# Kernel tuning notes

Measured on AMD Instinct MI355X. Metric: run time of the kernel, lower is better.

The kernel has to match this reference:

```python
import jax, jax.numpy as jnp
import numpy as np

DIM = 256; K = 3; PAD = 1; DIL = 1; B = 16; H = 56; W = 56
SP = 8           # share_planes
RADIX = 2
ATTN = max(DIM * RADIX // 4, 32)   # 128
EMB = K * K * DIM // SP            # 288

def conv(x, w, pad=0, dil=1, groups=1):
    return jax.lax.conv_general_dilated(
        x, w, (1, 1), [(pad, pad), (pad, pad)], rhs_dilation=(dil, dil),
        feature_group_count=groups, dimension_numbers=('NCHW', 'OIHW', 'NCHW'))

def bn(x, g, b, m, v, eps=1e-5):
    # eval-mode BatchNorm2d
    s = g * jax.lax.rsqrt(v + eps)
    return x * s[None, :, None, None] + (b - m * s)[None, :, None, None]

def gn(x, g, b, groups, eps=1e-5):
    Bb, C, Hh, Ww = x.shape
    xg = x.reshape(Bb, groups, C // groups, Hh, Ww)
    mu = xg.mean((2, 3, 4), keepdims=True)
    var = xg.var((2, 3, 4), keepdims=True)
    xg = (xg - mu) * jax.lax.rsqrt(var + eps)
    return xg.reshape(Bb, C, Hh, Ww) * g[None, :, None, None] + b[None, :, None, None]

def unfold3(x):
    # im2col for 3x3, stride 1, pad 1 -> (B, C, K*K, H, W)
    Bb, C, Hh, Ww = x.shape
    p = (K - 1) // 2
    xp = jnp.pad(x, ((0, 0), (0, 0), (p, p), (p, p)))
    return jnp.stack([xp[:, :, i:i + Hh, j:j + Ww] for i in range(K) for j in range(K)], axis=2)

def reference(x, ke_w, ke_g, ke_b, ke_m, ke_v, e1_w, e1_g, e1_b, e1_m, e1_v,
              e2_w, e2_b, gng, gnb, c1_w, c1_g, c1_b, c1_m, c1_v,
              b2_g, b2_b, b2_m, b2_v, s1_w, s1_b, s1_g, s1_bb, s1_m, s1_v,
              s2_w, s2_b):
    Bb = x.shape[0]
    # key embed: grouped kxk conv + BN + ReLU
    k = jax.nn.relu(bn(conv(x, ke_w, pad=PAD, dil=DIL, groups=4), ke_g, ke_b, ke_m, ke_v))
    qk = jnp.concatenate([x, k], axis=1)                     # (B, 2*DIM, H, W)
    # dynamic kernel branch
    wemb = jax.nn.relu(bn(conv(qk, e1_w), e1_g, e1_b, e1_m, e1_v))
    wemb = conv(wemb, e2_w) + e2_b[None, :, None, None]
    wemb = gn(wemb, gng, gnb, DIM // SP)                     # GroupNorm(dim//8 groups)
    wemb = wemb.reshape(Bb, DIM // SP, K * K, H, W)
    # value branch
    xq = bn(conv(x, c1_w), c1_g, c1_b, c1_m, c1_v)
    # local dynamic convolution: per-pixel kernel shared across SP channels
    patches = unfold3(xq).reshape(Bb, DIM // SP, SP, K * K, H, W)
    y = (patches * wemb[:, :, None]).sum(3).reshape(Bb, DIM, H, W)
    y = bn(y, b2_g, b2_b, b2_m, b2_v)
    y = y * jax.nn.sigmoid(y)                                # swish
    # split attention over radix=2 branches (y, k)
    xs = jnp.stack([y, k], axis=2)                           # (B, C, 2, H, W)
    gap = xs.sum(2).mean((2, 3), keepdims=True)              # (B, C, 1, 1)
    a = jax.nn.relu(bn(conv(gap, s1_w) + s1_b[None, :, None, None], s1_g, s1_bb, s1_m, s1_v))
    a = conv(a, s2_w) + s2_b[None, :, None, None]            # (B, 2*C, 1, 1)
    a = jax.nn.softmax(a.reshape(Bb, DIM, RADIX), axis=2)
    out = (xs * a[:, :, :, None, None]).sum(2)
    return out

def setup_inputs():
    key = jax.random.key(0)
    ks = iter(jax.random.split(key, 40))
    def n(shape, s=1.0):
        return jax.random.normal(next(ks), shape, jnp.float32) * s
    def u(shape):
        return jax.random.uniform(next(ks), shape, jnp.float32, minval=0.5, maxval=1.5)
    d = {}
    d['x'] = n((B, DIM, H, W))
    d['ke_w'] = n((DIM, DIM // 4, K, K), 0.05)
    d['ke_g'] = u((DIM,)); d['ke_b'] = n((DIM,), 0.1); d['ke_m'] = n((DIM,), 0.1); d['ke_v'] = u((DIM,))
    d['e1_w'] = n((DIM // 2, 2 * DIM, 1, 1), 0.05)
    d['e1_g'] = u((DIM // 2,)); d['e1_b'] = n((DIM // 2,), 0.1); d['e1_m'] = n((DIM // 2,), 0.1); d['e1_v'] = u((DIM // 2,))
    d['e2_w'] = n((EMB, DIM // 2, 1, 1), 0.05); d['e2_b'] = n((EMB,), 0.1)
    d['gng'] = u((EMB,)); d['gnb'] = n((EMB,), 0.1)
    d['c1_w'] = n((DIM, DIM, 1, 1), 0.05)
    d['c1_g'] = u((DIM,)); d['c1_b'] = n((DIM,), 0.1); d['c1_m'] = n((DIM,), 0.1); d['c1_v'] = u((DIM,))
    d['b2_g'] = u((DIM,)); d['b2_b'] = n((DIM,), 0.1); d['b2_m'] = n((DIM,), 0.1); d['b2_v'] = u((DIM,))
    d['s1_w'] = n((ATTN, DIM, 1, 1), 0.05); d['s1_b'] = n((ATTN,), 0.1)
    d['s1_g'] = u((ATTN,)); d['s1_bb'] = n((ATTN,), 0.1); d['s1_m'] = n((ATTN,), 0.1); d['s1_v'] = u((ATTN,))
    d['s2_w'] = n((RADIX * DIM, ATTN, 1, 1), 0.05); d['s2_b'] = n((RADIX * DIM,), 0.1)
    return d
```

## Files before the change

### kernel.cpp

```cpp
#include <hip/hip_runtime.h>
#include <hip/hip_bf16.h>

typedef __hip_bfloat16 bf16;
typedef float f32x4 __attribute__((ext_vector_type(4)));
typedef short s16x8 __attribute__((ext_vector_type(8)));

#define NPIX 3136
#define HDIM 56
#define CDIM 256

static __device__ __forceinline__ float b2f(bf16 v){ return __bfloat162float(v); }
static __device__ __forceinline__ bf16  f2b(float v){ return __float2bfloat16(v); }

#define O_KE_S 0
#define O_KE_B 256
#define O_E1_S 512
#define O_E1_B 640
#define O_C1_S 768
#define O_C1_B 1024
#define O_B2_S 1280
#define O_B2_B 1536
#define O_S1_S 1792
#define O_S1_B 1920
#define O_E2B  2048
#define O_GN_MU 2336
#define O_GN_RS 2848
#define O_GAP   3360
#define O_ATT   7456

__global__ void fold_params(
    const float* keg, const float* keb, const float* kem, const float* kev,
    const float* e1g, const float* e1b, const float* e1m, const float* e1v,
    const float* e2b,
    const float* c1g, const float* c1b, const float* c1m, const float* c1v,
    const float* b2g, const float* b2b, const float* b2m, const float* b2v,
    const float* s1g, const float* s1bb, const float* s1m, const float* s1v,
    float* o)
{
    int t = threadIdx.x;
    const float eps = 1e-5f;
    if (t < 256) {
        float s = keg[t] * rsqrtf(kev[t] + eps);
        o[O_KE_S + t] = s; o[O_KE_B + t] = keb[t] - kem[t] * s;
        s = c1g[t] * rsqrtf(c1v[t] + eps);
        o[O_C1_S + t] = s; o[O_C1_B + t] = c1b[t] - c1m[t] * s;
        s = b2g[t] * rsqrtf(b2v[t] + eps);
        o[O_B2_S + t] = s; o[O_B2_B + t] = b2b[t] - b2m[t] * s;
    }
    if (t < 128) {
        float s = e1g[t] * rsqrtf(e1v[t] + eps);
        o[O_E1_S + t] = s; o[O_E1_B + t] = e1b[t] - e1m[t] * s;
        s = s1g[t] * rsqrtf(s1v[t] + eps);
        o[O_S1_S + t] = s; o[O_S1_B + t] = s1bb[t] - s1m[t] * s;
    }
    if (t < 288) o[O_E2B + t] = e2b[t];
}

__global__ void zero_gap(float* gap) { gap[blockIdx.x * 256 + threadIdx.x] = 0.f; }

__global__ void cvt_w(const float* __restrict__ src, bf16* __restrict__ dst, int n)
{
    int i = blockIdx.x * 256 + threadIdx.x;
    if (i < n) dst[i] = f2b(src[i]);
}

__global__ void make_kewT(const float* __restrict__ kew, bf16* __restrict__ dst)
{
    int i = blockIdx.x * 256 + threadIdx.x;
    int ci = i & 63, co_l = (i >> 6) & 63;
    int gt = i >> 12;
    int tap = gt % 9, g = gt / 9;
    int co = g * 64 + co_l;
    dst[i] = f2b(kew[(co * 64 + ci) * 9 + tap]);
}

__global__ __launch_bounds__(256) void cvt_x(const float* __restrict__ x, bf16* __restrict__ xh)
{
    int b = blockIdx.y;
    int p0 = blockIdx.x * 64;
    __shared__ bf16 T[64][264];
    int t = threadIdx.x;
    for (int it = 0; it < 16; it++) {
        int slot = t + it * 256;
        int c = slot >> 4, ch4 = slot & 15;
        float4 v = *(const float4*)(x + ((long)b * CDIM + c) * NPIX + p0 + ch4 * 4);
        T[ch4 * 4 + 0][c] = f2b(v.x);
        T[ch4 * 4 + 1][c] = f2b(v.y);
        T[ch4 * 4 + 2][c] = f2b(v.z);
        T[ch4 * 4 + 3][c] = f2b(v.w);
    }
    __syncthreads();
    for (int it = 0; it < 8; it++) {
        int slot = t + it * 256;
        int p = slot >> 5, cc = slot & 31;
        *(float4*)(xh + ((long)b * NPIX + p0 + p) * CDIM + cc * 8) = *(const float4*)&T[p][cc * 8];
    }
}

__global__ __launch_bounds__(256) void gconv_mfma(
    const bf16* __restrict__ xh, const bf16* __restrict__ wT,
    const float* __restrict__ scale, const float* __restrict__ bias,
    bf16* __restrict__ kh)
{
    int b = blockIdx.z, g = blockIdx.y;
    int p0 = blockIdx.x * 64;
    __shared__ bf16 As[64][72];
    __shared__ bf16 Bs[64][72];
    int t = threadIdx.x;
    int wv = t >> 6, lane = t & 63, q = lane >> 4, ln = lane & 15;
    f32x4 acc[4] = {};
    for (int tap = 0; tap < 9; tap++) {
        int dh = tap / 3 - 1, dw = tap % 3 - 1;
        __syncthreads();
        #pragma unroll
        for (int i = 0; i < 2; i++) {
            int slot = t + i * 256;
            int row = slot >> 3, cc = slot & 7;
            int p = p0 + row, h = p / HDIM, w = p % HDIM;
            int h2 = h + dh, w2 = w + dw;
            float4 v = {0.f, 0.f, 0.f, 0.f};
            if ((unsigned)h2 < HDIM && (unsigned)w2 < HDIM)
                v = *(const float4*)(xh + ((long)b * NPIX + h2 * HDIM + w2) * CDIM + g * 64 + cc * 8);
            *(float4*)&As[row][cc * 8] = v;
            *(float4*)&Bs[row][cc * 8] = *(const float4*)(wT + ((long)(g * 9 + tap) * 64 + row) * 64 + cc * 8);
        }
        __syncthreads();
        #pragma unroll
        for (int ks = 0; ks < 2; ks++) {
            s16x8 a = *(const s16x8*)&As[wv * 16 + ln][ks * 32 + q * 8];
            #pragma unroll
            for (int s = 0; s < 4; s++) {
                s16x8 bb = *(const s16x8*)&Bs[s * 16 + ln][ks * 32 + q * 8];
                acc[s] = __builtin_amdgcn_mfma_f32_16x16x32_bf16(a, bb, acc[s], 0, 0, 0);
            }
        }
    }
    __syncthreads();
    #pragma unroll
    for (int s = 0; s < 4; s++) {
        int co = g * 64 + s * 16 + ln;
        float sc = scale[co], bi = bias[co];
        #pragma unroll
        for (int r = 0; r < 4; r++) {
            float v = fmaxf(acc[s][r] * sc + bi, 0.f);
            As[wv * 16 + q * 4 + r][s * 16 + ln] = f2b(v);
        }
    }
    __syncthreads();
    #pragma unroll
    for (int i = 0; i < 2; i++) {
        int slot = t + i * 256;
        int row = slot >> 3, cc = slot & 7;
        *(float4*)(kh + ((long)b * NPIX + p0 + row) * CDIM + g * 64 + cc * 8) = *(const float4*)&As[row][cc * 8];
    }
}

template<int MODE>
__global__ __launch_bounds__(256) void mfma_gemm(
    const bf16* __restrict__ Wt, const bf16* __restrict__ X0, const bf16* __restrict__ X1,
    int C0, int C1, int M,
    const float* __restrict__ scale, const float* __restrict__ bias,
    bf16* __restrict__ Y)
{
    int K = C0 + C1;
    int b = blockIdx.z;
    int p0 = blockIdx.x * 64;
    int m0 = blockIdx.y * 64;
    __shared__ bf16 As[64][72];
    __shared__ bf16 Bs[64][72];
    int t = threadIdx.x;
    int wv = t >> 6, lane = t & 63, q = lane >> 4, ln = lane & 15;
    f32x4 acc[4] = {};
    for (int k0 = 0; k0 < K; k0 += 64) {
        __syncthreads();
        #pragma unroll
        for (int i = 0; i < 2; i++) {
            int slot = t + i * 256;
            int row = slot >> 3, cc = slot & 7;
            int ch = k0 + cc * 8;
            const bf16* src;
            if (ch < C0) src = X0 + ((long)b * NPIX + p0 + row) * C0 + ch;
            else         src = X1 + ((long)b * NPIX + p0 + row) * C1 + (ch - C0);
            *(float4*)&As[row][cc * 8] = *(const float4*)src;

            int m = m0 + row;
            float4 v = {0.f, 0.f, 0.f, 0.f};
            if (m < M) v = *(const float4*)(Wt + (long)m * K + k0 + cc * 8);
            *(float4*)&Bs[row][cc * 8] = v;
        }
        __syncthreads();
        #pragma unroll
        for (int ks = 0; ks < 2; ks++) {
            s16x8 a = *(const s16x8*)&As[wv * 16 + ln][ks * 32 + q * 8];
            #pragma unroll
            for (int s = 0; s < 4; s++) {
                s16x8 bb = *(const s16x8*)&Bs[s * 16 + ln][ks * 32 + q * 8];
                acc[s] = __builtin_amdgcn_mfma_f32_16x16x32_bf16(a, bb, acc[s], 0, 0, 0);
            }
        }
    }
    __syncthreads();
    #pragma unroll
    for (int s = 0; s < 4; s++) {
        int m = m0 + s * 16 + ln;
        float sc = 1.f, bi;
        if (MODE == 0 || MODE == 2) { sc = scale[m]; bi = bias[m]; }
        else bi = bias[m];
        #pragma unroll
        for (int r = 0; r < 4; r++) {
            float v = acc[s][r] * sc + bi;
            if (MODE == 0) v = fmaxf(v, 0.f);
            As[wv * 16 + q * 4 + r][s * 16 + ln] = f2b(v);
        }
    }
    __syncthreads();
    #pragma unroll
    for (int i = 0; i < 2; i++) {
        int slot = t + i * 256;
        int row = slot >> 3, cc = slot & 7;
        if (m0 + cc * 8 + 8 <= M)
            *(float4*)(Y + ((long)b * NPIX + p0 + row) * M + m0 + cc * 8) = *(const float4*)&As[row][cc * 8];
    }
}

__global__ void gnstats(const bf16* __restrict__ wemb, float* __restrict__ mu_o, float* __restrict__ rs_o)
{
    int bg = blockIdx.x;
    int b = bg >> 5, grp = bg & 31;
    const bf16* base = wemb + (long)b * NPIX * 288 + grp * 9;
    float s = 0.f, sq = 0.f;
    for (int p = threadIdx.x; p < NPIX; p += 256) {
        const bf16* e = base + (long)p * 288;
        #pragma unroll
        for (int j = 0; j < 9; j++) { float v = b2f(e[j]); s += v; sq += v * v; }
    }
    __shared__ float ss[256], sb[256];
    int t = threadIdx.x;
    ss[t] = s; sb[t] = sq;
    __syncthreads();
    for (int o = 128; o > 0; o >>= 1) {
        if (t < o) { ss[t] += ss[t + o]; sb[t] += sb[t + o]; }
        __syncthreads();
    }
    if (t == 0) {
        float m = ss[0] / 28224.f;
        float var = sb[0] / 28224.f - m * m;
        mu_o[bg] = m; rs_o[bg] = rsqrtf(fmaxf(var, 0.f) + 1e-5f);
    }
}

__global__ __launch_bounds__(256) void dynconv(
    const bf16* __restrict__ xq, const bf16* __restrict__ wemb,
    const float* __restrict__ gmu, const float* __restrict__ grs,
    const float* __restrict__ gng, const float* __restrict__ gnb,
    const float* __restrict__ b2s, const float* __restrict__ b2b,
    bf16* __restrict__ y)
{
    int id = blockIdx.x * 256 + threadIdx.x;
    int grp = id & 31;
    int p = (id >> 5) % NPIX;
    int b = id / (NPIX * 32);
    int h = p / HDIM, w = p % HDIM;
    float mu = gmu[b * 32 + grp], rs = grs[b * 32 + grp];
    const bf16* wp = wemb + ((long)b * NPIX + p) * 288 + grp * 9;
    float wv[9];
    #pragma unroll
    for (int tp = 0; tp < 9; tp++)
        wv[tp] = (b2f(wp[tp]) - mu) * rs * gng[grp * 9 + tp] + gnb[grp * 9 + tp];
    float acc[8] = {};
    #pragma unroll
    for (int tp = 0; tp < 9; tp++) {
        int h2 = h + tp / 3 - 1, w2 = w + tp % 3 - 1;
        if ((unsigned)h2 >= HDIM || (unsigned)w2 >= HDIM) continue;
        const bf16* xp = xq + ((long)b * NPIX + h2 * HDIM + w2) * CDIM + grp * 8;
        s16x8 xv = *(const s16x8*)xp;
        const bf16* xb = (const bf16*)&xv;
        float wt = wv[tp];
        #pragma unroll
        for (int i = 0; i < 8; i++) acc[i] += b2f(xb[i]) * wt;
    }
    bf16 outv[8];
    #pragma unroll
    for (int i = 0; i < 8; i++) {
        int c = grp * 8 + i;
        float v = acc[i] * b2s[c] + b2b[c];
        outv[i] = f2b(v / (1.f + __expf(-v)));
    }
    *(float4*)(y + ((long)b * NPIX + p) * CDIM + grp * 8) = *(const float4*)outv;
}

__global__ void gapk(const bf16* __restrict__ y, const bf16* __restrict__ k, float* __restrict__ gap)
{
    int b = blockIdx.x, chunk = blockIdx.y, c = threadIdx.x;
    float s = 0.f;
    for (int i = 0; i < 64; i++) {
        long off = ((long)b * NPIX + chunk * 64 + i) * CDIM + c;
        s += b2f(y[off]) + b2f(k[off]);
    }
    atomicAdd(&gap[b * 256 + c], s * (1.f / NPIX));
}

__global__ void attnk(const float* __restrict__ gap,
                      const float* __restrict__ s1w, const float* __restrict__ s1b,
                      const float* __restrict__ s1s, const float* __restrict__ s1bi,
                      const float* __restrict__ s2w, const float* __restrict__ s2b,
                      float* __restrict__ att)
{
    int b = blockIdx.x, t = threadIdx.x;
    __shared__ float g[256], a1[128];
    for (int i = t; i < 256; i += 128) g[i] = gap[b * 256 + i];
    __syncthreads();
    float s = 0.f;
    for (int ci = 0; ci < 256; ci++) s += s1w[t * 256 + ci] * g[ci];
    s += s1b[t];
    s = s * s1s[t] + s1bi[t];
    a1[t] = fmaxf(s, 0.f);
    __syncthreads();
    for (int c = t; c < 256; c += 128) {
        float v0 = s2b[2 * c], v1 = s2b[2 * c + 1];
        for (int ci = 0; ci < 128; ci++) {
            float av = a1[ci];
            v0 += s2w[(2 * c) * 128 + ci] * av;
            v1 += s2w[(2 * c + 1) * 128 + ci] * av;
        }
        float m = fmaxf(v0, v1);
        float e0 = __expf(v0 - m), e1 = __expf(v1 - m);
        float inv = 1.f / (e0 + e1);
        att[(b * 256 + c) * 2 + 0] = e0 * inv;
        att[(b * 256 + c) * 2 + 1] = e1 * inv;
    }
}

__global__ __launch_bounds__(256) void finalk(
    const bf16* __restrict__ y, const bf16* __restrict__ k,
    const float* __restrict__ att, float* __restrict__ out)
{
    int b = blockIdx.z, c0 = blockIdx.y * 64, p0 = blockIdx.x * 64;
    __shared__ bf16 Ys[64][72], Ks[64][72];
    int t = threadIdx.x;
    #pragma unroll
    for (int i = 0; i < 2; i++) {
        int slot = t + i * 256;
        int row = slot >> 3, cc = slot & 7;
        long off = ((long)b * NPIX + p0 + row) * CDIM + c0 + cc * 8;
        *(float4*)&Ys[row][cc * 8] = *(const float4*)(y + off);
        *(float4*)&Ks[row][cc * 8] = *(const float4*)(k + off);
    }
    __syncthreads();
    int c_l = t >> 2, pc = t & 3;
    int c = c0 + c_l;
    float a0 = att[(b * 256 + c) * 2], a1 = att[(b * 256 + c) * 2 + 1];
    float4 o[4];
    float* of = (float*)o;
    #pragma unroll
    for (int j = 0; j < 16; j++) {
        int p = pc * 16 + j;
        of[j] = b2f(Ys[p][c_l]) * a0 + b2f(Ks[p][c_l]) * a1;
    }
    float* dst = out + ((long)b * CDIM + c) * NPIX + p0 + pc * 16;
    #pragma unroll
    for (int j = 0; j < 4; j++) ((float4*)dst)[j] = o[j];
}

extern "C" void kernel_launch(void* const* d_in, const int* in_sizes, int n_in,
                              void* d_out, int out_size, void* d_ws, size_t ws_size,
                              hipStream_t stream)
{
    const float* x    = (const float*)d_in[0];
    const float* ke_w = (const float*)d_in[1];
    const float* ke_g = (const float*)d_in[2];
    const float* ke_b = (const float*)d_in[3];
    const float* ke_m = (const float*)d_in[4];
    const float* ke_v = (const float*)d_in[5];
    const float* e1_w = (const float*)d_in[6];
    const float* e1_g = (const float*)d_in[7];
    const float* e1_b = (const float*)d_in[8];
    const float* e1_m = (const float*)d_in[9];
    const float* e1_v = (const float*)d_in[10];
    const float* e2_w = (const float*)d_in[11];
    const float* e2_b = (const float*)d_in[12];
    const float* gng  = (const float*)d_in[13];
    const float* gnb  = (const float*)d_in[14];
    const float* c1_w = (const float*)d_in[15];
    const float* c1_g = (const float*)d_in[16];
    const float* c1_b = (const float*)d_in[17];
    const float* c1_m = (const float*)d_in[18];
    const float* c1_v = (const float*)d_in[19];
    const float* b2_g = (const float*)d_in[20];
    const float* b2_b = (const float*)d_in[21];
    const float* b2_m = (const float*)d_in[22];
    const float* b2_v = (const float*)d_in[23];
    const float* s1_w = (const float*)d_in[24];
    const float* s1_b = (const float*)d_in[25];
    const float* s1_g = (const float*)d_in[26];
    const float* s1_bb= (const float*)d_in[27];
    const float* s1_m = (const float*)d_in[28];
    const float* s1_v = (const float*)d_in[29];
    const float* s2_w = (const float*)d_in[30];
    const float* s2_b = (const float*)d_in[31];

    float* fold = (float*)d_ws;
    bf16* wsb   = (bf16*)((char*)d_ws + 65536);
    bf16* xh   = wsb;
    bf16* kh   = xh + 12845056L;
    bf16* wemb = kh + 12845056L;
    bf16* w1   = wemb + 14450688L;
    bf16* xq   = w1;
    bf16* yb   = xh;
    bf16* kewT = w1 + 12845056L;
    bf16* e1wb = kewT + 147456L;
    bf16* e2wb = e1wb + 65536L;
    bf16* c1wb = e2wb + 36864L;

    fold_params<<<dim3(1), dim3(512), 0, stream>>>(
        ke_g, ke_b, ke_m, ke_v, e1_g, e1_b, e1_m, e1_v, e2_b,
        c1_g, c1_b, c1_m, c1_v, b2_g, b2_b, b2_m, b2_v,
        s1_g, s1_bb, s1_m, s1_v, fold);

    zero_gap<<<dim3(16), dim3(256), 0, stream>>>(fold + O_GAP);

    cvt_w<<<dim3(256), dim3(256), 0, stream>>>(e1_w, e1wb, 65536);
    cvt_w<<<dim3(144), dim3(256), 0, stream>>>(e2_w, e2wb, 36864);
    cvt_w<<<dim3(256), dim3(256), 0, stream>>>(c1_w, c1wb, 65536);
    make_kewT<<<dim3(576), dim3(256), 0, stream>>>(ke_w, kewT);

    cvt_x<<<dim3(49, 16), dim3(256), 0, stream>>>(x, xh);

    gconv_mfma<<<dim3(49, 4, 16), dim3(256), 0, stream>>>(
        xh, kewT, fold + O_KE_S, fold + O_KE_B, kh);

    mfma_gemm<0><<<dim3(49, 2, 16), dim3(256), 0, stream>>>(
        e1wb, xh, kh, 256, 256, 128, fold + O_E1_S, fold + O_E1_B, w1);

    mfma_gemm<1><<<dim3(49, 5, 16), dim3(256), 0, stream>>>(
        e2wb, w1, (const bf16*)nullptr, 128, 0, 288, (const float*)nullptr, fold + O_E2B, wemb);

    gnstats<<<dim3(512), dim3(256), 0, stream>>>(wemb, fold + O_GN_MU, fold + O_GN_RS);

    mfma_gemm<2><<<dim3(49, 4, 16), dim3(256), 0, stream>>>(
        c1wb, xh, (const bf16*)nullptr, 256, 0, 256, fold + O_C1_S, fold + O_C1_B, xq);

    dynconv<<<dim3(6272), dim3(256), 0, stream>>>(
        xq, wemb, fold + O_GN_MU, fold + O_GN_RS, gng, gnb,
        fold + O_B2_S, fold + O_B2_B, yb);

    gapk<<<dim3(16, 49), dim3(256), 0, stream>>>(yb, kh, fold + O_GAP);

    attnk<<<dim3(16), dim3(128), 0, stream>>>(
        fold + O_GAP, s1_w, s1_b, fold + O_S1_S, fold + O_S1_B, s2_w, s2_b, fold + O_ATT);

    finalk<<<dim3(49, 4, 16), dim3(256), 0, stream>>>(yb, kh, fold + O_ATT, (float*)d_out);
}
```

Baseline: 390.8 us.

## Fuse prep kernels, halo-tile grouped conv, direct-load GEMMs, fold GN stats into GEMM

Merges the parameter folding, weight conversion and zeroing launches into one prep kernel. The grouped 3x3 conv now loads a halo tile of input rows once into shared memory and reuses it across all nine taps, reading weights directly from global memory. The 1x1 GEMMs drop shared-memory staging and read A and B fragments straight from global memory. GroupNorm sums are accumulated with atomics in the e2 GEMM epilogue, which removes the separate gnstats pass. The costs are uncoalesced global fragment loads, atomic contention, and a less stable sum/sumsq variance computed in fp32.

Measured after the change: 498.6 us. 27.6% more time.

```diff
diff --git a/kernel.cpp b/kernel.cpp
--- a/kernel.cpp
+++ b/kernel.cpp
@@ -23,55 +23,57 @@
 #define O_S1_S 1792
 #define O_S1_B 1920
 #define O_E2B  2048
-#define O_GN_MU 2336
-#define O_GN_RS 2848
-#define O_GAP   3360
-#define O_ATT   7456
-
-__global__ void fold_params(
+#define O_GNS  2336
+#define O_GAP  3360
+#define O_ATT  7456
+
+__global__ void prep(
+    const float* __restrict__ kew, const float* __restrict__ e1w,
+    const float* __restrict__ e2w, const float* __restrict__ c1w,
     const float* keg, const float* keb, const float* kem, const float* kev,
     const float* e1g, const float* e1b, const float* e1m, const float* e1v,
     const float* e2b,
     const float* c1g, const float* c1b, const float* c1m, const float* c1v,
     const float* b2g, const float* b2b, const float* b2m, const float* b2v,
     const float* s1g, const float* s1bb, const float* s1m, const float* s1v,
-    float* o)
-{
-    int t = threadIdx.x;
-    const float eps = 1e-5f;
-    if (t < 256) {
-        float s = keg[t] * rsqrtf(kev[t] + eps);
-        o[O_KE_S + t] = s; o[O_KE_B + t] = keb[t] - kem[t] * s;
-        s = c1g[t] * rsqrtf(c1v[t] + eps);
-        o[O_C1_S + t] = s; o[O_C1_B + t] = c1b[t] - c1m[t] * s;
-        s = b2g[t] * rsqrtf(b2v[t] + eps);
-        o[O_B2_S + t] = s; o[O_B2_B + t] = b2b[t] - b2m[t] * s;
-    }
-    if (t < 128) {
-        float s = e1g[t] * rsqrtf(e1v[t] + eps);
-        o[O_E1_S + t] = s; o[O_E1_B + t] = e1b[t] - e1m[t] * s;
-        s = s1g[t] * rsqrtf(s1v[t] + eps);
-        o[O_S1_S + t] = s; o[O_S1_B + t] = s1bb[t] - s1m[t] * s;
-    }
-    if (t < 288) o[O_E2B + t] = e2b[t];
-}
-
-__global__ void zero_gap(float* gap) { gap[blockIdx.x * 256 + threadIdx.x] = 0.f; }
-
-__global__ void cvt_w(const float* __restrict__ src, bf16* __restrict__ dst, int n)
-{
-    int i = blockIdx.x * 256 + threadIdx.x;
-    if (i < n) dst[i] = f2b(src[i]);
-}
-
-__global__ void make_kewT(const float* __restrict__ kew, bf16* __restrict__ dst)
-{
-    int i = blockIdx.x * 256 + threadIdx.x;
-    int ci = i & 63, co_l = (i >> 6) & 63;
-    int gt = i >> 12;
-    int tap = gt % 9, g = gt / 9;
-    int co = g * 64 + co_l;
-    dst[i] = f2b(kew[(co * 64 + ci) * 9 + tap]);
+    bf16* kewT, bf16* e1wb, bf16* e2wb, bf16* c1wb, float* o)
+{
+    int bid = blockIdx.x, t = threadIdx.x;
+    if (bid < 576) {
+        int i = bid * 256 + t;
+        int ci = i & 63, co_l = (i >> 6) & 63;
+        int gt = i >> 12;
+        int tap = gt % 9, g = gt / 9;
+        int co = g * 64 + co_l;
+        kewT[i] = f2b(kew[(co * 64 + ci) * 9 + tap]);
+    } else if (bid < 832) {
+        int i = (bid - 576) * 256 + t; e1wb[i] = f2b(e1w[i]);
+    } else if (bid < 976) {
+        int i = (bid - 832) * 256 + t; e2wb[i] = f2b(e2w[i]);
+    } else if (bid < 1232) {
+        int i = (bid - 976) * 256 + t; c1wb[i] = f2b(c1w[i]);
+    } else if (bid == 1232) {
+        const float eps = 1e-5f;
+        {
+            float s = keg[t] * rsqrtf(kev[t] + eps);
+            o[O_KE_S + t] = s; o[O_KE_B + t] = keb[t] - kem[t] * s;
+            s = c1g[t] * rsqrtf(c1v[t] + eps);
+            o[O_C1_S + t] = s; o[O_C1_B + t] = c1b[t] - c1m[t] * s;
+            s = b2g[t] * rsqrtf(b2v[t] + eps);
+            o[O_B2_S + t] = s; o[O_B2_B + t] = b2b[t] - b2m[t] * s;
+        }
+        if (t < 128) {
+            float s = e1g[t] * rsqrtf(e1v[t] + eps);
+            o[O_E1_S + t] = s; o[O_E1_B + t] = e1b[t] - e1m[t] * s;
+            s = s1g[t] * rsqrtf(s1v[t] + eps);
+            o[O_S1_S + t] = s; o[O_S1_B + t] = s1bb[t] - s1m[t] * s;
+        }
+        for (int i = t; i < 288; i += 256) o[O_E2B + i] = e2b[i];
+    } else {
+        int j = (bid - 1233) * 256 + t;
+        if (j < 1024) o[O_GNS + j] = 0.f;
+        else          o[O_GAP + j - 1024] = 0.f;
+    }
 }
 
 __global__ __launch_bounds__(256) void cvt_x(const float* __restrict__ x, bf16* __restrict__ xh)
@@ -104,113 +106,128 @@
 {
     int b = blockIdx.z, g = blockIdx.y;
     int p0 = blockIdx.x * 64;
-    __shared__ bf16 As[64][72];
-    __shared__ bf16 Bs[64][72];
+    __shared__ bf16 As[5 * 58 * 72];
     int t = threadIdx.x;
     int wv = t >> 6, lane = t & 63, q = lane >> 4, ln = lane & 15;
+    int r_first = p0 / HDIM - 1;
+
+    #pragma unroll
+    for (int i = 0; i < 10; i++) {
+        int slot = t + i * 256;
+        if (slot < 2320) {
+            int chunk = slot & 7, pos = slot >> 3;
+            int ri = pos / 58, ci = pos - ri * 58;
+            int h = r_first + ri, w = ci - 1;
+            float4 v = {0.f, 0.f, 0.f, 0.f};
+            if ((unsigned)h < HDIM && (unsigned)w < HDIM)
+                v = *(const float4*)(xh + ((long)b * NPIX + h * HDIM + w) * CDIM + g * 64 + chunk * 8);
+            *(float4*)&As[pos * 72 + chunk * 8] = v;
+        }
+    }
+    __syncthreads();
+
+    int posp[4];
+    #pragma unroll
+    for (int pt = 0; pt < 4; pt++) {
+        int p = p0 + pt * 16 + ln;
+        int hp = p / HDIM, wp = p - hp * HDIM;
+        posp[pt] = (hp - r_first) * 58 + wp + 1;
+    }
+    const bf16* wbase = wT + ((long)(g * 9) * 64 + wv * 16 + ln) * 64;
+
     f32x4 acc[4] = {};
+    #pragma unroll
     for (int tap = 0; tap < 9; tap++) {
-        int dh = tap / 3 - 1, dw = tap % 3 - 1;
-        __syncthreads();
+        int dpos = (tap / 3 - 1) * 58 + (tap % 3 - 1);
+        const bf16* wp = wbase + tap * 64 * 64;
+        s16x8 B0 = *(const s16x8*)(wp + q * 8);
+        s16x8 B1 = *(const s16x8*)(wp + 32 + q * 8);
         #pragma unroll
-        for (int i = 0; i < 2; i++) {
-            int slot = t + i * 256;
-            int row = slot >> 3, cc = slot & 7;
-            int p = p0 + row, h = p / HDIM, w = p % HDIM;
-            int h2 = h + dh, w2 = w + dw;
-            float4 v = {0.f, 0.f, 0.f, 0.f};
-            if ((unsigned)h2 < HDIM && (unsigned)w2 < HDIM)
-                v = *(const float4*)(xh + ((long)b * NPIX + h2 * HDIM + w2) * CDIM + g * 64 + cc * 8);
-            *(float4*)&As[row][cc * 8] = v;
-            *(float4*)&Bs[row][cc * 8] = *(const float4*)(wT + ((long)(g * 9 + tap) * 64 + row) * 64 + cc * 8);
-        }
-        __syncthreads();
+        for (int pt = 0; pt < 4; pt++) {
+            int base = (posp[pt] + dpos) * 72 + q * 8;
+            s16x8 a0 = *(const s16x8*)&As[base];
+            s16x8 a1 = *(const s16x8*)&As[base + 32];
+            acc[pt] = __builtin_amdgcn_mfma_f32_16x16x32_bf16(a0, B0, acc[pt], 0, 0, 0);
+            acc[pt] = __builtin_amdgcn_mfma_f32_16x16x32_bf16(a1, B1, acc[pt], 0, 0, 0);
+        }
+    }
+
+    __syncthreads();
+    int co = g * 64 + wv * 16 + ln;
+    float sc = scale[co], bi = bias[co];
+    #pragma unroll
+    for (int pt = 0; pt < 4; pt++)
         #pragma unroll
-        for (int ks = 0; ks < 2; ks++) {
-            s16x8 a = *(const s16x8*)&As[wv * 16 + ln][ks * 32 + q * 8];
-            #pragma unroll
-            for (int s = 0; s < 4; s++) {
-                s16x8 bb = *(const s16x8*)&Bs[s * 16 + ln][ks * 32 + q * 8];
-                acc[s] = __builtin_amdgcn_mfma_f32_16x16x32_bf16(a, bb, acc[s], 0, 0, 0);
-            }
-        }
-    }
-    __syncthreads();
-    #pragma unroll
-    for (int s = 0; s < 4; s++) {
-        int co = g * 64 + s * 16 + ln;
-        float sc = scale[co], bi = bias[co];
-        #pragma unroll
-        for (int r = 0; r < 4; r++) {
-            float v = fmaxf(acc[s][r] * sc + bi, 0.f);
-            As[wv * 16 + q * 4 + r][s * 16 + ln] = f2b(v);
-        }
-    }
+        for (int r = 0; r < 4; r++)
+            As[(pt * 16 + q * 4 + r) * 72 + wv * 16 + ln] = f2b(fmaxf(acc[pt][r] * sc + bi, 0.f));
     __syncthreads();
     #pragma unroll
     for (int i = 0; i < 2; i++) {
         int slot = t + i * 256;
         int row = slot >> 3, cc = slot & 7;
-        *(float4*)(kh + ((long)b * NPIX + p0 + row) * CDIM + g * 64 + cc * 8) = *(const float4*)&As[row][cc * 8];
+        *(float4*)(kh + ((long)b * NPIX + p0 + row) * CDIM + g * 64 + cc * 8) = *(const float4*)&As[row * 72 + cc * 8];
     }
 }
 
 template<int MODE>
 __global__ __launch_bounds__(256) void mfma_gemm(
     const bf16* __restrict__ Wt, const bf16* __restrict__ X0, const bf16* __restrict__ X1,
-    int C0, int C1, int M,
+    int C0, int K, int M,
     const float* __restrict__ scale, const float* __restrict__ bias,
-    bf16* __restrict__ Y)
-{
-    int K = C0 + C1;
+    bf16* __restrict__ Y, float* __restrict__ gnsum)
+{
     int b = blockIdx.z;
     int p0 = blockIdx.x * 64;
     int m0 = blockIdx.y * 64;
-    __shared__ bf16 As[64][72];
-    __shared__ bf16 Bs[64][72];
+    __shared__ bf16 T[64 * 72];
+    __shared__ float gs[64];
     int t = threadIdx.x;
     int wv = t >> 6, lane = t & 63, q = lane >> 4, ln = lane & 15;
+    if (MODE == 1) { if (t < 64) gs[t] = 0.f; __syncthreads(); }
+
+    int px = p0 + wv * 16 + ln;
+    const bf16* pA0 = X0 + ((long)b * NPIX + px) * C0;
+    const bf16* pA1 = X1 ? X1 + ((long)b * NPIX + px) * (K - C0) : nullptr;
+    const bf16* pB[4];
+    #pragma unroll
+    for (int s = 0; s < 4; s++) {
+        int m = m0 + s * 16 + ln; if (m > M - 1) m = M - 1;
+        pB[s] = Wt + (long)m * K;
+    }
+
     f32x4 acc[4] = {};
     for (int k0 = 0; k0 < K; k0 += 64) {
-        __syncthreads();
+        const bf16* pa = (k0 < C0) ? (pA0 + k0) : (pA1 + (k0 - C0));
+        s16x8 a0 = *(const s16x8*)(pa + q * 8);
+        s16x8 a1 = *(const s16x8*)(pa + 32 + q * 8);
         #pragma unroll
-        for (int i = 0; i < 2; i++) {
-            int slot = t + i * 256;
-            int row = slot >> 3, cc = slot & 7;
-            int ch = k0 + cc * 8;
-            const bf16* src;
-            if (ch < C0) src = X0 + ((long)b * NPIX + p0 + row) * C0 + ch;
-            else         src = X1 + ((long)b * NPIX + p0 + row) * C1 + (ch - C0);
-            *(float4*)&As[row][cc * 8] = *(const float4*)src;
-
-            int m = m0 + row;
-            float4 v = {0.f, 0.f, 0.f, 0.f};
-            if (m < M) v = *(const float4*)(Wt + (long)m * K + k0 + cc * 8);
-            *(float4*)&Bs[row][cc * 8] = v;
-        }
-        __syncthreads();
-        #pragma unroll
-        for (int ks = 0; ks < 2; ks++) {
-            s16x8 a = *(const s16x8*)&As[wv * 16 + ln][ks * 32 + q * 8];
-            #pragma unroll
-            for (int s = 0; s < 4; s++) {
-                s16x8 bb = *(const s16x8*)&Bs[s * 16 + ln][ks * 32 + q * 8];
-                acc[s] = __builtin_amdgcn_mfma_f32_16x16x32_bf16(a, bb, acc[s], 0, 0, 0);
-            }
-        }
-    }
-    __syncthreads();
+        for (int s = 0; s < 4; s++) {
+            s16x8 b0 = *(const s16x8*)(pB[s] + k0 + q * 8);
+            s16x8 b1 = *(const s16x8*)(pB[s] + k0 + 32 + q * 8);
+            acc[s] = __builtin_amdgcn_mfma_f32_16x16x32_bf16(a0, b0, acc[s], 0, 0, 0);
+            acc[s] = __builtin_amdgcn_mfma_f32_16x16x32_bf16(a1, b1, acc[s], 0, 0, 0);
+        }
+    }
+
     #pragma unroll
     for (int s = 0; s < 4; s++) {
         int m = m0 + s * 16 + ln;
+        int mc = (m > M - 1) ? (M - 1) : m;
         float sc = 1.f, bi;
-        if (MODE == 0 || MODE == 2) { sc = scale[m]; bi = bias[m]; }
-        else bi = bias[m];
+        if (MODE == 0 || MODE == 2) { sc = scale[mc]; bi = bias[mc]; }
+        else bi = bias[mc];
+        float ps = 0.f, pq = 0.f;
         #pragma unroll
         for (int r = 0; r < 4; r++) {
             float v = acc[s][r] * sc + bi;
             if (MODE == 0) v = fmaxf(v, 0.f);
-            As[wv * 16 + q * 4 + r][s * 16 + ln] = f2b(v);
+            if (MODE == 1) { ps += v; pq += v * v; }
+            T[(wv * 16 + q * 4 + r) * 72 + s * 16 + ln] = f2b(v);
+        }
+        if (MODE == 1 && m < M) {
+            int grp = m / 9;
+            atomicAdd(&gs[grp * 2], ps);
+            atomicAdd(&gs[grp * 2 + 1], pq);
         }
     }
     __syncthreads();
@@ -219,39 +236,14 @@
         int slot = t + i * 256;
         int row = slot >> 3, cc = slot & 7;
         if (m0 + cc * 8 + 8 <= M)
-            *(float4*)(Y + ((long)b * NPIX + p0 + row) * M + m0 + cc * 8) = *(const float4*)&As[row][cc * 8];
-    }
-}
-
-__global__ void gnstats(const bf16* __restrict__ wemb, float* __restrict__ mu_o, float* __restrict__ rs_o)
-{
-    int bg = blockIdx.x;
-    int b = bg >> 5, grp = bg & 31;
-    const bf16* base = wemb + (long)b * NPIX * 288 + grp * 9;
-    float s = 0.f, sq = 0.f;
-    for (int p = threadIdx.x; p < NPIX; p += 256) {
-        const bf16* e = base + (long)p * 288;
-        #pragma unroll
-        for (int j = 0; j < 9; j++) { float v = b2f(e[j]); s += v; sq += v * v; }
-    }
-    __shared__ float ss[256], sb[256];
-    int t = threadIdx.x;
-    ss[t] = s; sb[t] = sq;
-    __syncthreads();
-    for (int o = 128; o > 0; o >>= 1) {
-        if (t < o) { ss[t] += ss[t + o]; sb[t] += sb[t + o]; }
-        __syncthreads();
-    }
-    if (t == 0) {
-        float m = ss[0] / 28224.f;
-        float var = sb[0] / 28224.f - m * m;
-        mu_o[bg] = m; rs_o[bg] = rsqrtf(fmaxf(var, 0.f) + 1e-5f);
-    }
+            *(float4*)(Y + ((long)b * NPIX + p0 + row) * M + m0 + cc * 8) = *(const float4*)&T[row * 72 + cc * 8];
+    }
+    if (MODE == 1 && t < 64) atomicAdd(&gnsum[b * 64 + t], gs[t]);
 }
 
 __global__ __launch_bounds__(256) void dynconv(
     const bf16* __restrict__ xq, const bf16* __restrict__ wemb,
-    const float* __restrict__ gmu, const float* __restrict__ grs,
+    const float* __restrict__ gnsum,
     const float* __restrict__ gng, const float* __restrict__ gnb,
     const float* __restrict__ b2s, const float* __restrict__ b2b,
     bf16* __restrict__ y)
@@ -261,7 +253,10 @@
     int p = (id >> 5) % NPIX;
     int b = id / (NPIX * 32);
     int h = p / HDIM, w = p % HDIM;
-    float mu = gmu[b * 32 + grp], rs = grs[b * 32 + grp];
+    float S = gnsum[b * 64 + grp * 2], Q = gnsum[b * 64 + grp * 2 + 1];
+    float mu = S * (1.f / 28224.f);
+    float var = Q * (1.f / 28224.f) - mu * mu;
+    float rs = rsqrtf(fmaxf(var, 0.f) + 1e-5f);
     const bf16* wp = wemb + ((long)b * NPIX + p) * 288 + grp * 9;
     float wv[9];
     #pragma unroll
@@ -412,17 +407,12 @@
     bf16* e2wb = e1wb + 65536L;
     bf16* c1wb = e2wb + 36864L;
 
-    fold_params<<<dim3(1), dim3(512), 0, stream>>>(
+    prep<<<dim3(1253), dim3(256), 0, stream>>>(
+        ke_w, e1_w, e2_w, c1_w,
         ke_g, ke_b, ke_m, ke_v, e1_g, e1_b, e1_m, e1_v, e2_b,
         c1_g, c1_b, c1_m, c1_v, b2_g, b2_b, b2_m, b2_v,
-        s1_g, s1_bb, s1_m, s1_v, fold);
-
-    zero_gap<<<dim3(16), dim3(256), 0, stream>>>(fold + O_GAP);
-
-    cvt_w<<<dim3(256), dim3(256), 0, stream>>>(e1_w, e1wb, 65536);
-    cvt_w<<<dim3(144), dim3(256), 0, stream>>>(e2_w, e2wb, 36864);
-    cvt_w<<<dim3(256), dim3(256), 0, stream>>>(c1_w, c1wb, 65536);
-    make_kewT<<<dim3(576), dim3(256), 0, stream>>>(ke_w, kewT);
+        s1_g, s1_bb, s1_m, s1_v,
+        kewT, e1wb, e2wb, c1wb, fold);
 
     cvt_x<<<dim3(49, 16), dim3(256), 0, stream>>>(x, xh);
 
@@ -430,18 +420,17 @@
         xh, kewT, fold + O_KE_S, fold + O_KE_B, kh);
 
     mfma_gemm<0><<<dim3(49, 2, 16), dim3(256), 0, stream>>>(
-        e1wb, xh, kh, 256, 256, 128, fold + O_E1_S, fold + O_E1_B, w1);
+        e1wb, xh, kh, 256, 512, 128, fold + O_E1_S, fold + O_E1_B, w1, nullptr);
 
     mfma_gemm<1><<<dim3(49, 5, 16), dim3(256), 0, stream>>>(
-        e2wb, w1, (const bf16*)nullptr, 128, 0, 288, (const float*)nullptr, fold + O_E2B, wemb);
-
-    gnstats<<<dim3(512), dim3(256), 0, stream>>>(wemb, fold + O_GN_MU, fold + O_GN_RS);
+        e2wb, w1, (const bf16*)nullptr, 128, 128, 288, (const float*)nullptr, fold + O_E2B,
+        wemb, fold + O_GNS);
 
     mfma_gemm<2><<<dim3(49, 4, 16), dim3(256), 0, stream>>>(
-        c1wb, xh, (const bf16*)nullptr, 256, 0, 256, fold + O_C1_S, fold + O_C1_B, xq);
+        c1wb, xh, (const bf16*)nullptr, 256, 256, 256, fold + O_C1_S, fold + O_C1_B, xq, nullptr);
 
     dynconv<<<dim3(6272), dim3(256), 0, stream>>>(
-        xq, wemb, fold + O_GN_MU, fold + O_GN_RS, gng, gnb,
+        xq, wemb, fold + O_GNS, gng, gnb,
         fold + O_B2_S, fold + O_B2_B, yb);
 
     gapk<<<dim3(16, 49), dim3(256), 0, stream>>>(yb, kh, fold + O_GAP);
```
